# Kernel optimization log

Hardware: AMD Instinct MI355X
Metric: run time of the kernel (lower is better)

## Reference

```python
import jax, jax.numpy as jnp
import numpy as np

THRESHOLD = 0.5

def setup_inputs() -> dict:
    key = jax.random.key(0)
    k1, k2 = jax.random.split(key)
    N, F, B = 800000, 64, 8
    xs = jax.random.uniform(k1, (N, 1), dtype=jnp.float32)          # scores in [0,1)
    pl = jax.random.normal(k2, (N, F), dtype=jnp.float32)           # payload features
    rs = (jnp.arange(B + 1, dtype=jnp.int32) * (N // B))            # row splits [0,100k,...,800k]
    return {"xs": xs, "pl": pl, "rs": rs}

def reference(xs, pl, rs):
    # SelectThreshold(xs, pl, rs, threshold=0.5):
    #   keep rows with score > threshold, compact features, recompute row splits,
    #   and emit scatter indices (original row ids of the kept rows).
    # JIT-static variant: kept rows are stably compacted to the front of an
    # [N, F] buffer; slots >= n_sel are zero-padded, scatter idx padded with N.
    N = pl.shape[0]
    B = rs.shape[0] - 1
    mask = xs[:, 0] > THRESHOLD                                      # [N] bool
    # stable argsort: selected rows first, original (per-segment) order preserved
    order = jnp.argsort(jnp.logical_not(mask))                       # [N] int
    n_sel = jnp.sum(mask.astype(jnp.int32))
    valid = jnp.arange(N) < n_sel                                    # [N] bool
    newfeat = jnp.where(valid[:, None], pl[order], jnp.zeros((), pl.dtype))  # [N, F]
    scatter_idxs = jnp.where(valid, order, N).astype(jnp.int32)[:, None]     # [N, 1]
    # per-event selected counts -> new row splits
    seg_ids = jnp.searchsorted(rs, jnp.arange(N, dtype=rs.dtype), side='right') - 1  # [N]
    counts = jax.ops.segment_sum(mask.astype(rs.dtype), seg_ids, num_segments=B)     # [B]
    new_rs = jnp.concatenate([jnp.zeros((1,), rs.dtype), jnp.cumsum(counts)])        # [B+1]
    return newfeat, new_rs, scatter_idxs
```

## Files before the change

### kernel.cpp

```cpp
#include <hip/hip_runtime.h>


#define THRESH 0.5f
#define RPB 1024

__global__ void k_count(const float* __restrict__ xs, int N,
                        int* __restrict__ ranks, int* __restrict__ blk_counts) {
    __shared__ int wc[4][4];
    const int tid  = threadIdx.x;
    const int lane = tid & 63, wave = tid >> 6;
    const int base = blockIdx.x * RPB;
    int running = 0;
    for (int c = 0; c < 4; ++c) {
        int i = base + c * 256 + tid;
        int m = (i < N) && (xs[i] > THRESH);
        unsigned long long bal = __ballot(m);
        if (lane == 0) wc[c][wave] = __popcll(bal);
        __syncthreads();
        int waveoff = 0, tot = 0;
        for (int w = 0; w < 4; ++w) { int v = wc[c][w]; if (w < wave) waveoff += v; tot += v; }
        int pre = running + waveoff + (int)__popcll(bal & ((1ull << lane) - 1ull));
        if (i < N) ranks[i] = (pre << 1) | m;
        running += tot;
    }
    if (tid == 0) blk_counts[blockIdx.x] = running;
}

__global__ void k_scan(const int* __restrict__ blk_counts, int nblocks,
                       const int* __restrict__ ranks,
                       const int* __restrict__ rs, int nrs, int N,
                       int* __restrict__ blk_off, int* __restrict__ nsel_out,
                       float* __restrict__ out_rs) {
    __shared__ int s[1024];
    __shared__ int s_total;
    const int t = threadIdx.x;
    int v = (t < nblocks) ? blk_counts[t] : 0;
    s[t] = v;
    __syncthreads();
    for (int d = 1; d < 1024; d <<= 1) {
        int add = (t >= d) ? s[t - d] : 0;
        __syncthreads();
        s[t] += add;
        __syncthreads();
    }
    int excl = s[t] - v;
    if (t < nblocks) blk_off[t] = excl;
    if (t == 1023) s_total = s[t];
    __syncthreads();
    int n_sel = s_total;
    if (t == 0) nsel_out[0] = n_sel;
    if (t < nrs) {
        int j = rs[t];
        int val;
        if (j >= N)      val = n_sel;
        else if (j <= 0) val = 0;
        else             val = blk_off[j >> 10] + (ranks[j] >> 1);
        out_rs[t] = (float)val;
    }
}

__global__ void k_scatter_gather(const int* __restrict__ ranks,
                                 const int* __restrict__ blk_off,
                                 const int* __restrict__ nsel,
                                 const float4* __restrict__ pl4, int N,
                                 float4* __restrict__ outf4,
                                 float* __restrict__ out_sc) {
    int tid = blockIdx.x * blockDim.x + threadIdx.x;
    int i = tid >> 4;
    int c = tid & 15;
    if (i >= N) return;
    const int ns = nsel[0];
    const int e  = ranks[i];
    if (e & 1) {
        int r = blk_off[i >> 10] + (e >> 1);
        float4 v = pl4[(size_t)i * 16 + c];
        outf4[(size_t)r * 16 + c] = v;
        if (c == 0) out_sc[r] = (float)i;
    }
    if (i >= ns) {
        outf4[(size_t)i * 16 + c] = make_float4(0.f, 0.f, 0.f, 0.f);
        if (c == 0) out_sc[i] = (float)N;
    }
}

extern "C" void kernel_launch(void* const* d_in, const int* in_sizes, int n_in,
                              void* d_out, int out_size, void* d_ws, size_t ws_size,
                              hipStream_t stream) {
    const float* xs = (const float*)d_in[0];
    const float* pl = (const float*)d_in[1];
    const int*   rs = (const int*)d_in[2];
    const int N   = in_sizes[0];
    const int F   = in_sizes[1] / N;
    const int nrs = in_sizes[2];

    float* out      = (float*)d_out;
    float* out_feat = out;
    float* out_rs   = out + (size_t)N * F;
    float* out_sc   = out_rs + nrs;

    int* ranks      = (int*)d_ws;
    int* blk_counts = ranks + N;
    int* blk_off    = blk_counts + 1024;
    int* nsel       = blk_off + 1024;

    const int nblocks = (N + RPB - 1) / RPB;

    k_count<<<nblocks, 256, 0, stream>>>(xs, N, ranks, blk_counts);
    k_scan <<<1,       1024, 0, stream>>>(blk_counts, nblocks, ranks, rs, nrs, N,
                                          blk_off, nsel, out_rs);
    k_scatter_gather<<<(N * 16 + 255) / 256, 256, 0, stream>>>(
        ranks, blk_off, nsel, (const float4*)pl, N, (float4*)out_feat, out_sc);
}
```

Measured before the change: 343.3 us.

## Fuse count and block scan via last-block atomic, vectorize mask, nontemporal copies

```diff
diff --git a/kernel.cpp b/kernel.cpp
--- a/kernel.cpp
+++ b/kernel.cpp
@@ -4,66 +4,104 @@
 #define THRESH 0.5f
 #define RPB 1024
 
-__global__ void k_count(const float* __restrict__ xs, int N,
-                        int* __restrict__ ranks, int* __restrict__ blk_counts) {
-    __shared__ int wc[4][4];
+typedef float f4 __attribute__((ext_vector_type(4)));
+
+__global__ void k_count_scan(const float* __restrict__ xs, int N, int nblocks,
+                             const int* __restrict__ rs, int nrs,
+                             int* __restrict__ ranks, int* __restrict__ blk_counts,
+                             unsigned* __restrict__ ctr,
+                             int* __restrict__ blk_off, int* __restrict__ nsel_out,
+                             float* __restrict__ out_rs) {
+    __shared__ int s_wave[4];
+    __shared__ int s_flag;
+    __shared__ int s_tot;
+    __shared__ int s_boff[1024];
     const int tid  = threadIdx.x;
     const int lane = tid & 63, wave = tid >> 6;
-    const int base = blockIdx.x * RPB;
-    int running = 0;
-    for (int c = 0; c < 4; ++c) {
-        int i = base + c * 256 + tid;
-        int m = (i < N) && (xs[i] > THRESH);
-        unsigned long long bal = __ballot(m);
-        if (lane == 0) wc[c][wave] = __popcll(bal);
-        __syncthreads();
-        int waveoff = 0, tot = 0;
-        for (int w = 0; w < 4; ++w) { int v = wc[c][w]; if (w < wave) waveoff += v; tot += v; }
-        int pre = running + waveoff + (int)__popcll(bal & ((1ull << lane) - 1ull));
-        if (i < N) ranks[i] = (pre << 1) | m;
-        running += tot;
+    const int idx4 = blockIdx.x * 256 + tid;
+    const int row0 = idx4 * 4;
+
+    int m0 = 0, m1 = 0, m2 = 0, m3 = 0;
+    if (row0 + 3 < N) {
+        f4 v = *reinterpret_cast<const f4*>(&xs[row0]);
+        m0 = v.x > THRESH; m1 = v.y > THRESH; m2 = v.z > THRESH; m3 = v.w > THRESH;
+    } else if (row0 < N) {
+        m0 = xs[row0] > THRESH;
+        if (row0 + 1 < N) m1 = xs[row0 + 1] > THRESH;
+        if (row0 + 2 < N) m2 = xs[row0 + 2] > THRESH;
     }
-    if (tid == 0) blk_counts[blockIdx.x] = running;
-}
+    int cnt = m0 + m1 + m2 + m3;
 
-__global__ void k_scan(const int* __restrict__ blk_counts, int nblocks,
-                       const int* __restrict__ ranks,
-                       const int* __restrict__ rs, int nrs, int N,
-                       int* __restrict__ blk_off, int* __restrict__ nsel_out,
-                       float* __restrict__ out_rs) {
-    __shared__ int s[1024];
-    __shared__ int s_total;
-    const int t = threadIdx.x;
-    int v = (t < nblocks) ? blk_counts[t] : 0;
-    s[t] = v;
+    int inc = cnt;
+    #pragma unroll
+    for (int d = 1; d < 64; d <<= 1) { int u = __shfl_up(inc, d); if (lane >= d) inc += u; }
+    if (lane == 63) s_wave[wave] = inc;
     __syncthreads();
-    for (int d = 1; d < 1024; d <<= 1) {
-        int add = (t >= d) ? s[t - d] : 0;
-        __syncthreads();
-        s[t] += add;
-        __syncthreads();
+    int waveoff = 0, total = 0;
+    #pragma unroll
+    for (int w = 0; w < 4; ++w) { int t = s_wave[w]; if (w < wave) waveoff += t; total += t; }
+    int pre = waveoff + inc - cnt;
+
+    if (row0 + 3 < N) {
+        int4 e;
+        e.x = (pre << 1) | m0;
+        e.y = ((pre + m0) << 1) | m1;
+        e.z = ((pre + m0 + m1) << 1) | m2;
+        e.w = ((pre + m0 + m1 + m2) << 1) | m3;
+        *reinterpret_cast<int4*>(&ranks[row0]) = e;
+    } else if (row0 < N) {
+        ranks[row0] = (pre << 1) | m0;
+        if (row0 + 1 < N) ranks[row0 + 1] = ((pre + m0) << 1) | m1;
+        if (row0 + 2 < N) ranks[row0 + 2] = ((pre + m0 + m1) << 1) | m2;
     }
-    int excl = s[t] - v;
-    if (t < nblocks) blk_off[t] = excl;
-    if (t == 1023) s_total = s[t];
+
     __syncthreads();
-    int n_sel = s_total;
-    if (t == 0) nsel_out[0] = n_sel;
-    if (t < nrs) {
-        int j = rs[t];
+    if (tid == 0) {
+        blk_counts[blockIdx.x] = total;
+        __threadfence();
+        unsigned old = atomicAdd(ctr, 1u);
+        s_flag = (old == (unsigned)(nblocks - 1));
+    }
+    __syncthreads();
+    if (!s_flag) return;
+
+    __threadfence();
+    int c[4]; const int base = tid * 4;
+    #pragma unroll
+    for (int k = 0; k < 4; ++k) c[k] = (base + k < nblocks) ? blk_counts[base + k] : 0;
+    int tsum = c[0] + c[1] + c[2] + c[3];
+    int tinc = tsum;
+    #pragma unroll
+    for (int d = 1; d < 64; d <<= 1) { int u = __shfl_up(tinc, d); if (lane >= d) tinc += u; }
+    if (lane == 63) s_wave[wave] = tinc;
+    __syncthreads();
+    int woff = 0, gtot = 0;
+    #pragma unroll
+    for (int w = 0; w < 4; ++w) { int t = s_wave[w]; if (w < wave) woff += t; gtot += t; }
+    int excl = woff + tinc - tsum;
+    #pragma unroll
+    for (int k = 0; k < 4; ++k) {
+        s_boff[base + k] = excl;
+        if (base + k < nblocks) blk_off[base + k] = excl;
+        excl += c[k];
+    }
+    if (tid == 0) { nsel_out[0] = gtot; s_tot = gtot; }
+    __syncthreads();
+    if (tid < nrs) {
+        int j = rs[tid];
         int val;
-        if (j >= N)      val = n_sel;
+        if (j >= N)      val = s_tot;
         else if (j <= 0) val = 0;
-        else             val = blk_off[j >> 10] + (ranks[j] >> 1);
-        out_rs[t] = (float)val;
+        else             val = s_boff[j >> 10] + (ranks[j] >> 1);
+        out_rs[tid] = (float)val;
     }
 }
 
 __global__ void k_scatter_gather(const int* __restrict__ ranks,
                                  const int* __restrict__ blk_off,
                                  const int* __restrict__ nsel,
-                                 const float4* __restrict__ pl4, int N,
-                                 float4* __restrict__ outf4,
+                                 const f4* __restrict__ pl4, int N,
+                                 f4* __restrict__ outf4,
                                  float* __restrict__ out_sc) {
     int tid = blockIdx.x * blockDim.x + threadIdx.x;
     int i = tid >> 4;
@@ -73,12 +111,13 @@
     const int e  = ranks[i];
     if (e & 1) {
         int r = blk_off[i >> 10] + (e >> 1);
-        float4 v = pl4[(size_t)i * 16 + c];
-        outf4[(size_t)r * 16 + c] = v;
+        f4 v = __builtin_nontemporal_load(&pl4[(size_t)i * 16 + c]);
+        __builtin_nontemporal_store(v, &outf4[(size_t)r * 16 + c]);
         if (c == 0) out_sc[r] = (float)i;
     }
     if (i >= ns) {
-        outf4[(size_t)i * 16 + c] = make_float4(0.f, 0.f, 0.f, 0.f);
+        f4 z = {0.f, 0.f, 0.f, 0.f};
+        __builtin_nontemporal_store(z, &outf4[(size_t)i * 16 + c]);
         if (c == 0) out_sc[i] = (float)N;
     }
 }
@@ -102,12 +141,15 @@
     int* blk_counts = ranks + N;
     int* blk_off    = blk_counts + 1024;
     int* nsel       = blk_off + 1024;
+    unsigned* ctr   = (unsigned*)(nsel + 1);
 
     const int nblocks = (N + RPB - 1) / RPB;
 
-    k_count<<<nblocks, 256, 0, stream>>>(xs, N, ranks, blk_counts);
-    k_scan <<<1,       1024, 0, stream>>>(blk_counts, nblocks, ranks, rs, nrs, N,
-                                          blk_off, nsel, out_rs);
+    hipMemsetAsync(ctr, 0, sizeof(unsigned), stream);
+
+    k_count_scan<<<nblocks, 256, 0, stream>>>(xs, N, nblocks, rs, nrs,
+                                              ranks, blk_counts, ctr,
+                                              blk_off, nsel, out_rs);
     k_scatter_gather<<<(N * 16 + 255) / 256, 256, 0, stream>>>(
-        ranks, blk_off, nsel, (const float4*)pl, N, (float4*)out_feat, out_sc);
+        ranks, blk_off, nsel, (const f4*)pl, N, (f4*)out_feat, out_sc);
 }
```

New measurement: 354.6 us. 3.3% more time.
